# Kernel optimization log

Hardware: AMD Instinct MI355X
Metric: run time of the kernel (lower is better)

Reference implementation:

```python
import jax, jax.numpy as jnp
import numpy as np

N_HEAD = 16


def setup_inputs() -> dict:
    key = jax.random.key(0)
    ks = jax.random.split(key, 6)
    B, T, C = 8, 1024, 1024
    s = 0.02
    return {
        "x": jax.random.normal(ks[0], (B, T, C), dtype=jnp.float32),
        "Wk": jax.random.normal(ks[1], (C, C), dtype=jnp.float32) * s,
        "bk": jnp.zeros((C,), dtype=jnp.float32),
        "Wq": jax.random.normal(ks[2], (C, C), dtype=jnp.float32) * s,
        "bq": jnp.zeros((C,), dtype=jnp.float32),
        "Wv": jax.random.normal(ks[3], (C, C), dtype=jnp.float32) * s,
        "bv": jnp.zeros((C,), dtype=jnp.float32),
        "Wp": jax.random.normal(ks[4], (C, C), dtype=jnp.float32) * s,
        "bp": jnp.zeros((C,), dtype=jnp.float32),
    }


def reference(x, Wk, bk, Wq, bq, Wv, bv, Wp, bp):
    B, T, C = x.shape
    H = N_HEAD
    d = C // H
    # QKV projections, split heads -> [B, H, T, d]
    k = (x @ Wk + bk).reshape(B, T, H, d).transpose(0, 2, 1, 3)
    q = (x @ Wq + bq).reshape(B, T, H, d).transpose(0, 2, 1, 3)
    v = (x @ Wv + bv).reshape(B, T, H, d).transpose(0, 2, 1, 3)
    # NOTE: original computes K @ Q^T (not Q @ K^T) and scales by C^-0.5
    attn = jnp.einsum('bhid,bhjd->bhij', k, q) * (C ** -0.5)
    mask = jnp.tril(jnp.ones((T, T), dtype=bool))  # tril==0 positions masked
    attn = jnp.where(mask, attn, -jnp.inf)
    attn = jax.nn.softmax(attn, axis=-1)
    out = jnp.einsum('bhij,bhjd->bhid', attn, v)  # [B, H, T, d]
    out = out.transpose(0, 2, 1, 3).reshape(B, T, C)
    return out @ Wp + bp
```

## Files before the change

### kernel.cpp

```cpp
#include <hip/hip_runtime.h>

typedef unsigned short u16;
typedef unsigned int u32;
typedef __bf16 bf16x8 __attribute__((ext_vector_type(8)));
typedef float f32x4 __attribute__((ext_vector_type(4)));

__device__ __forceinline__ u16 f2bf(float f) {
  u32 u = __builtin_bit_cast(u32, f);
  u += 0x7fffu + ((u >> 16) & 1u);
  return (u16)(u >> 16);
}

#define GLOAD_LDS16(g, l) __builtin_amdgcn_global_load_lds( \
    (const __attribute__((address_space(1))) void*)(g),     \
    (__attribute__((address_space(3))) void*)(l), 16, 0, 0)

#define SCK (0.03125f * 1.44269504088896f)

#define BARF() do { asm volatile("" ::: "memory"); \
                    __builtin_amdgcn_s_barrier();  \
                    asm volatile("" ::: "memory"); } while (0)

__global__ __launch_bounds__(256) void cvt_x_k(const float* __restrict__ x,
                                               u16* __restrict__ xb) {
  size_t i = (size_t)blockIdx.x * 256 + threadIdx.x;
  const float4* p = reinterpret_cast<const float4*>(x) + i * 2;
  float4 a = p[0], b = p[1];
  u32 w0 = f2bf(a.x) | ((u32)f2bf(a.y) << 16);
  u32 w1 = f2bf(a.z) | ((u32)f2bf(a.w) << 16);
  u32 w2 = f2bf(b.x) | ((u32)f2bf(b.y) << 16);
  u32 w3 = f2bf(b.z) | ((u32)f2bf(b.w) << 16);
  uint4 o; o.x = w0; o.y = w1; o.z = w2; o.w = w3;
  *reinterpret_cast<uint4*>(xb + i * 8) = o;
}

__global__ __launch_bounds__(256) void transW_k(const float* __restrict__ W0,
                                                const float* __restrict__ W1,
                                                const float* __restrict__ W2,
                                                const float* __restrict__ W3,
                                                u16* __restrict__ WT) {
  __shared__ float tile[64][65];
  const float* W = blockIdx.z == 0 ? W0 : blockIdx.z == 1 ? W1
                 : blockIdx.z == 2 ? W2 : W3;
  u16* dst = WT + (size_t)blockIdx.z * 1024 * 1024;
  const int k0 = blockIdx.x * 64, n0 = blockIdx.y * 64;
  const int tid = threadIdx.x;
  const int rr = tid >> 4, c4 = (tid & 15) * 4;
#pragma unroll
  for (int p = 0; p < 4; ++p) {
    int r = rr + p * 16;
    float4 v = *reinterpret_cast<const float4*>(W + (size_t)(k0 + r) * 1024 + n0 + c4);
    tile[r][c4 + 0] = v.x; tile[r][c4 + 1] = v.y;
    tile[r][c4 + 2] = v.z; tile[r][c4 + 3] = v.w;
  }
  __syncthreads();
#pragma unroll
  for (int p = 0; p < 4; ++p) {
    int nl = rr + p * 16;
    u32 w0 = f2bf(tile[c4 + 0][nl]) | ((u32)f2bf(tile[c4 + 1][nl]) << 16);
    u32 w1 = f2bf(tile[c4 + 2][nl]) | ((u32)f2bf(tile[c4 + 3][nl]) << 16);
    uint2 o; o.x = w0; o.y = w1;
    *reinterpret_cast<uint2*>(dst + (size_t)(n0 + nl) * 1024 + k0 + c4) = o;
  }
}

template <int MODE>
__global__ __launch_bounds__(512, 2) void gemm8_k(
    const u16* __restrict__ A, const u16* __restrict__ BT,
    const float* __restrict__ bias0, const float* __restrict__ bias1,
    const float* __restrict__ bias2,
    u16* __restrict__ out_k, u16* __restrict__ out_q, u16* __restrict__ out_vT,
    float* __restrict__ out_f) {
  constexpr int BN = (MODE == 0) ? 192 : 128;
  constexpr int NB = BN / 64;
  constexpr int NBLO = NB - NB / 2;
  constexpr int NBHI = NB / 2;
  constexpr int LPT = 4 + NB;
  constexpr int WCW = BN / 4;

  __shared__ __align__(16) u16 As[2][256 * 64];
  __shared__ __align__(16) u16 Bs[2][BN * 64];

  const int tid = threadIdx.x;
  const int w = tid >> 6, lane = tid & 63;
  const int wr = w >> 2, wc = w & 3;
  const int fr = lane & 15, fq = lane >> 4;
  const int d = fr & 7;

  const int bid = (int)blockIdx.x;
  const int xcd = bid & 7, c = bid >> 3;
  int bx, by;
  if constexpr (MODE == 0) {
    bx = (xcd & 3) * 8 + (c >> 3);
    by = (xcd >> 2) * 8 + (c & 7);
  } else {
    bx = xcd * 4 + (c >> 3);
    by = c & 7;
  }
  const int row0 = bx * 256, col0 = by * BN;

  const int r0 = tid >> 3;
  const int cbg = (tid & 7) ^ (r0 & 7);
  const u16* Asrc = A + (size_t)(row0 + r0) * 1024 + cbg * 8;
  const u16* Bsrc = BT + (size_t)(col0 + r0) * 1024 + cbg * 8;

#define STAGE8(buf, t) do {                                                  \
    _Pragma("unroll")                                                        \
    for (int sw = 0; sw < 4; ++sw)                                           \
      GLOAD_LDS16(Asrc + (size_t)sw * 65536 + (t) * 64,                      \
                  &As[buf][sw * 4096 + tid * 8]);                            \
    _Pragma("unroll")                                                        \
    for (int sw = 0; sw < NB; ++sw)                                          \
      GLOAD_LDS16(Bsrc + (size_t)sw * 65536 + (t) * 64,                      \
                  &Bs[buf][sw * 4096 + tid * 8]);                            \
  } while (0)

#define AOFF(mb, kk) ((wr * 128 + (mb) * 16 + fr) * 128 + (((((kk) << 2) | fq) ^ d) << 4))
#define BOFF(nb, kk) ((wc * WCW + (nb) * 16 + fr) * 128 + (((((kk) << 2) | fq) ^ d) << 4))

  f32x4 acc[8][NB] = {};

  STAGE8(0, 0);
  STAGE8(1, 1);
  asm volatile("s_waitcnt vmcnt(%0)" :: "n"(LPT) : "memory");
  BARF();

#pragma unroll 1
  for (int g = 0; g < 16; ++g) {
    const int buf = g & 1;
    const char* Ac = (const char*)&As[buf][0];
    const char* Bc = (const char*)&Bs[buf][0];
    bf16x8 a03[4][2], a47[4][2], blo[NBLO][2], bhi[NBHI][2];

#pragma unroll
    for (int mb = 0; mb < 4; ++mb)
#pragma unroll
      for (int kk = 0; kk < 2; ++kk)
        a03[mb][kk] = *(const bf16x8*)(Ac + AOFF(mb, kk));
#pragma unroll
    for (int nb = 0; nb < NBLO; ++nb)
#pragma unroll
      for (int kk = 0; kk < 2; ++kk)
        blo[nb][kk] = *(const bf16x8*)(Bc + BOFF(nb, kk));
#pragma unroll
    for (int nb = 0; nb < NBHI; ++nb)
#pragma unroll
      for (int kk = 0; kk < 2; ++kk)
        bhi[nb][kk] = *(const bf16x8*)(Bc + BOFF(NBLO + nb, kk));
    asm volatile("s_waitcnt lgkmcnt(%0)" :: "n"(2 * NBHI) : "memory");
    __builtin_amdgcn_s_setprio(1);
#pragma unroll
    for (int mb = 0; mb < 4; ++mb)
#pragma unroll
      for (int nb = 0; nb < NBLO; ++nb)
#pragma unroll
        for (int kk = 0; kk < 2; ++kk)
          acc[mb][nb] = __builtin_amdgcn_mfma_f32_16x16x32_bf16(
              a03[mb][kk], blo[nb][kk], acc[mb][nb], 0, 0, 0);
    __builtin_amdgcn_s_setprio(0);
    BARF();

#pragma unroll
    for (int mb = 0; mb < 4; ++mb)
#pragma unroll
      for (int kk = 0; kk < 2; ++kk)
        a47[mb][kk] = *(const bf16x8*)(Ac + AOFF(4 + mb, kk));
    asm volatile("s_waitcnt lgkmcnt(8)" ::: "memory");
    __builtin_amdgcn_s_setprio(1);
#pragma unroll
    for (int mb = 0; mb < 4; ++mb)
#pragma unroll
      for (int nb = 0; nb < NBHI; ++nb)
#pragma unroll
        for (int kk = 0; kk < 2; ++kk)
          acc[mb][NBLO + nb] = __builtin_amdgcn_mfma_f32_16x16x32_bf16(
              a03[mb][kk], bhi[nb][kk], acc[mb][NBLO + nb], 0, 0, 0);
    __builtin_amdgcn_s_setprio(0);
    BARF();

    asm volatile("s_waitcnt lgkmcnt(0)" ::: "memory");
    __builtin_amdgcn_s_setprio(1);
#pragma unroll
    for (int mb = 0; mb < 4; ++mb)
#pragma unroll
      for (int nb = 0; nb < NBHI; ++nb)
#pragma unroll
        for (int kk = 0; kk < 2; ++kk)
          acc[4 + mb][NBLO + nb] = __builtin_amdgcn_mfma_f32_16x16x32_bf16(
              a47[mb][kk], bhi[nb][kk], acc[4 + mb][NBLO + nb], 0, 0, 0);
    __builtin_amdgcn_s_setprio(0);
    BARF();

    if (g + 2 < 16) STAGE8(buf, g + 2);
    __builtin_amdgcn_s_setprio(1);
#pragma unroll
    for (int mb = 0; mb < 4; ++mb)
#pragma unroll
      for (int nb = 0; nb < NBLO; ++nb)
#pragma unroll
        for (int kk = 0; kk < 2; ++kk)
          acc[4 + mb][nb] = __builtin_amdgcn_mfma_f32_16x16x32_bf16(
              a47[mb][kk], blo[nb][kk], acc[4 + mb][nb], 0, 0, 0);
    __builtin_amdgcn_s_setprio(0);
    if (g <= 13)      asm volatile("s_waitcnt vmcnt(%0)" :: "n"(LPT) : "memory");
    else if (g == 14) asm volatile("s_waitcnt vmcnt(0)" ::: "memory");
    BARF();
  }
#undef STAGE8
#undef AOFF
#undef BOFF

  if constexpr (MODE == 0) {
#pragma unroll
    for (int mb = 0; mb < 8; ++mb) {
#pragma unroll
      for (int nb = 0; nb < NB; ++nb) {
        const int rg = row0 + wr * 128 + mb * 16 + fq * 4;
        const int cg = col0 + wc * WCW + nb * 16 + fr;
        const int which = cg >> 10;
        const int nloc = cg & 1023;
        const float bv = (which == 0 ? bias0 : which == 1 ? bias1 : bias2)[nloc];
        if (which == 0) {
#pragma unroll
          for (int r = 0; r < 4; ++r)
            out_k[(size_t)(rg + r) * 1024 + nloc] = f2bf((acc[mb][nb][r] + bv) * SCK);
        } else if (which == 1) {
#pragma unroll
          for (int r = 0; r < 4; ++r)
            out_q[(size_t)(rg + r) * 1024 + nloc] = f2bf(acc[mb][nb][r] + bv);
        } else {
          const int bb = rg >> 10, t = rg & 1023;
          const int hh = nloc >> 6, dl = nloc & 63;
          u32 w0 = f2bf(acc[mb][nb][0] + bv) | ((u32)f2bf(acc[mb][nb][1] + bv) << 16);
          u32 w1 = f2bf(acc[mb][nb][2] + bv) | ((u32)f2bf(acc[mb][nb][3] + bv) << 16);
          uint2 ov; ov.x = w0; ov.y = w1;
          *reinterpret_cast<uint2*>(out_vT + ((size_t)(bb * 16 + hh) * 64 + dl) * 1024 + t) = ov;
        }
      }
    }
  } else {
#pragma unroll
    for (int mb = 0; mb < 8; ++mb)
#pragma unroll
      for (int nb = 0; nb < NB; ++nb) {
        const int rg = row0 + wr * 128 + mb * 16 + fq * 4;
        const int cg = col0 + wc * WCW + nb * 16 + fr;
        const float bv = bias0[cg];
#pragma unroll
        for (int r = 0; r < 4; ++r)
          out_f[(size_t)(rg + r) * 1024 + cg] = acc[mb][nb][r] + bv;
      }
  }
}

__global__ __launch_bounds__(256, 4) void attn_k(const u16* __restrict__ Q,
                                                 const u16* __restrict__ K,
                                                 const u16* __restrict__ vT,
                                                 u16* __restrict__ O) {
  __shared__ __align__(16) u16 KsA[4096], KsB[4096], VsA[4096], VsB[4096];
  __shared__ __align__(16) u16 Plds[4][16][40];
  const int tid = threadIdx.x;
  const int w = tid >> 6, lane = tid & 63;
  const int fr = lane & 15, fq = lane >> 4, koff = fq * 8;

  const int n = blockIdx.x + 8 * (blockIdx.y + 16 * blockIdx.z);
  const int xcd = n & 7, rest = n >> 3;
  const int g = rest >> 3, pair = rest & 7;
  const int hb = xcd + 8 * g;
  const int h = hb & 15, b = hb >> 4;

  const size_t bstride = (size_t)1024 * 1024;
  const u16* Qb = Q + b * bstride + h * 64;
  const u16* Kg = K + b * bstride + h * 64;
  const u16* Vg = vT + ((size_t)(b * 16 + h) * 64) * 1024;

  const int srow = tid >> 3;
  const int scb = (tid & 7) ^ (srow & 7);
  const u16* KgT = Kg + (size_t)srow * 1024 + scb * 8;
  const u16* VgT = Vg + (size_t)srow * 1024 + scb * 8;

  const int vK0 = fr * 128 + ((fq ^ (fr & 7)) << 4);
  const int vK1 = vK0 ^ 64;
  const int pw = w * 1280 + fq * 320 + fr * 2;
  const int pr = w * 1280 + fr * 80 + fq * 16;

#define STAGE(KS, VS, jt) do {                                          \
    GLOAD_LDS16(KgT + (size_t)(jt) * 65536, &KS[tid * 8]);              \
    GLOAD_LDS16(KgT + (size_t)(jt) * 65536 + 32 * 1024, &KS[2048 + tid * 8]); \
    GLOAD_LDS16(VgT + (jt) * 64, &VS[tid * 8]);                         \
    GLOAD_LDS16(VgT + (jt) * 64 + 32 * 1024, &VS[2048 + tid * 8]);      \
  } while (0)

#pragma unroll 1
  for (int ph = 0; ph < 2; ++ph) {
    const int T = ph ? (15 - pair) : pair;
    const int i0 = T * 64;
    const int ibase = i0 + w * 16;

    bf16x8 aq0 = *reinterpret_cast<const bf16x8*>(&Qb[(size_t)(ibase + fr) * 1024 + koff]);
    bf16x8 aq1 = *reinterpret_cast<const bf16x8*>(&Qb[(size_t)(ibase + fr) * 1024 + koff + 32]);

    f32x4 o[4] = {};
    float lp[4] = {0.f, 0.f, 0.f, 0.f};

    auto compute = [&](const u16* KS, const u16* VS, bool diag) {
      const char* Kc = reinterpret_cast<const char*>(KS);
      const char* Vc = reinterpret_cast<const char*>(VS);
      f32x4 s[4];
#pragma unroll
      for (int jc = 0; jc < 4; ++jc) {
        bf16x8 bk0 = *reinterpret_cast<const bf16x8*>(Kc + vK0 + jc * 2048);
        bf16x8 bk1 = *reinterpret_cast<const bf16x8*>(Kc + vK1 + jc * 2048);
        f32x4 z = {};
        z = __builtin_amdgcn_mfma_f32_16x16x32_bf16(aq0, bk0, z, 0, 0, 0);
        s[jc] = __builtin_amdgcn_mfma_f32_16x16x32_bf16(aq1, bk1, z, 0, 0, 0);
      }
      bf16x8 bv0[4], bv1[4];
#pragma unroll
      for (int dn = 0; dn < 4; ++dn) {
        bv0[dn] = *reinterpret_cast<const bf16x8*>(Vc + vK0 + dn * 2048);
        bv1[dn] = *reinterpret_cast<const bf16x8*>(Vc + vK1 + dn * 2048);
      }
      float p[4][4];
      if (diag) {
#pragma unroll
        for (int r = 0; r < 4; ++r) {
          const int il = w * 16 + fq * 4 + r;
#pragma unroll
          for (int jc = 0; jc < 4; ++jc) {
            const int jl = jc * 16 + fr;
            p[jc][r] = (jl <= il) ? __builtin_amdgcn_exp2f(s[jc][r]) : 0.f;
          }
        }
      } else {
#pragma unroll
        for (int r = 0; r < 4; ++r)
#pragma unroll
          for (int jc = 0; jc < 4; ++jc)
            p[jc][r] = __builtin_amdgcn_exp2f(s[jc][r]);
      }
#pragma unroll
      for (int r = 0; r < 4; ++r)
        lp[r] += (p[0][r] + p[1][r]) + (p[2][r] + p[3][r]);
      char* Pc = reinterpret_cast<char*>(&Plds[0][0][0]);
#pragma unroll
      for (int jh = 0; jh < 2; ++jh) {
#pragma unroll
        for (int r = 0; r < 4; ++r)
#pragma unroll
          for (int j2 = 0; j2 < 2; ++j2)
            *reinterpret_cast<u16*>(Pc + pw + r * 80 + j2 * 32) = f2bf(p[jh * 2 + j2][r]);
        bf16x8 ap = *reinterpret_cast<const bf16x8*>(Pc + pr);
#pragma unroll
        for (int dn = 0; dn < 4; ++dn)
          o[dn] = __builtin_amdgcn_mfma_f32_16x16x32_bf16(ap, jh ? bv1[dn] : bv0[dn],
                                                          o[dn], 0, 0, 0);
      }
    };

    STAGE(KsA, VsA, 0);
    int t = 0;
    while (true) {
      {
        const bool more = t < T;
        if (more) STAGE(KsB, VsB, t + 1);
        if (more) { asm volatile("s_waitcnt vmcnt(4)" ::: "memory"); }
        else      { asm volatile("s_waitcnt vmcnt(0)" ::: "memory"); }
        __builtin_amdgcn_s_barrier();
        compute(KsA, VsA, t == T);
        __builtin_amdgcn_s_barrier();
        if (!more) break;
        ++t;
      }
      {
        const bool more = t < T;
        if (more) STAGE(KsA, VsA, t + 1);
        if (more) { asm volatile("s_waitcnt vmcnt(4)" ::: "memory"); }
        else      { asm volatile("s_waitcnt vmcnt(0)" ::: "memory"); }
        __builtin_amdgcn_s_barrier();
        compute(KsB, VsB, t == T);
        __builtin_amdgcn_s_barrier();
        if (!more) break;
        ++t;
      }
    }

#pragma unroll
    for (int x = 1; x < 16; x <<= 1)
#pragma unroll
      for (int r = 0; r < 4; ++r) lp[r] += __shfl_xor(lp[r], x);
#pragma unroll
    for (int r = 0; r < 4; ++r) {
      const float inv = 1.f / lp[r];
      const int ig = ibase + fq * 4 + r;
#pragma unroll
      for (int dn = 0; dn < 4; ++dn)
        O[((size_t)b * 1024 + ig) * 1024 + h * 64 + dn * 16 + fr] = f2bf(o[dn][r] * inv);
    }
  }
#undef STAGE
}

extern "C" void kernel_launch(void* const* d_in, const int* in_sizes, int n_in,
                              void* d_out, int out_size, void* d_ws, size_t ws_size,
                              hipStream_t stream) {
  const float* x  = (const float*)d_in[0];
  const float* Wk = (const float*)d_in[1];
  const float* bk = (const float*)d_in[2];
  const float* Wq = (const float*)d_in[3];
  const float* bq = (const float*)d_in[4];
  const float* Wv = (const float*)d_in[5];
  const float* bv = (const float*)d_in[6];
  const float* Wp = (const float*)d_in[7];
  const float* bp = (const float*)d_in[8];
  float* out = (float*)d_out;

  char* ws = (char*)d_ws;
  u16* xb   = (u16*)(ws);
  u16* WT   = (u16*)(ws + ((size_t)16 << 20));
  u16* kbuf = (u16*)(ws + ((size_t)24 << 20));
  u16* qbuf = (u16*)(ws + ((size_t)40 << 20));
  u16* vT   = (u16*)(ws + ((size_t)56 << 20));
  u16* aout = (u16*)(ws + ((size_t)72 << 20));

  cvt_x_k<<<4096, 256, 0, stream>>>(x, xb);
  transW_k<<<dim3(16, 16, 4), 256, 0, stream>>>(Wk, Wq, Wv, Wp, WT);
  gemm8_k<0><<<512, 512, 0, stream>>>(xb, WT, bk, bq, bv,
                                      kbuf, qbuf, vT, nullptr);
  attn_k<<<dim3(8, 16, 8), 256, 0, stream>>>(kbuf, qbuf, vT, aout);
  gemm8_k<1><<<256, 512, 0, stream>>>(aout, WT + (size_t)3 * 1024 * 1024,
                                      bp, nullptr, nullptr,
                                      nullptr, nullptr, nullptr, out);
}
```

Before: 138.4 us.

## Merge prep kernels into one launch and reorder GEMM MFMA phases by k-slice

Combines the x-to-bf16 conversion and weight transpose kernels into a single launch, using the block index to pick which job a block does. This removes one kernel launch and its gap. It also restructures the GEMM inner loop so each of the four barrier-separated phases covers a full k-half (kk=0 or kk=1) across all N blocks rather than splitting into lo/hi N halves. The new LDS load order and lgkmcnt waits are meant to overlap the fragment loads with the MFMAs differently, at the risk of longer stalls or higher register pressure.

```diff
diff --git a/kernel.cpp b/kernel.cpp
--- a/kernel.cpp
+++ b/kernel.cpp
@@ -21,30 +21,32 @@
                     __builtin_amdgcn_s_barrier();  \
                     asm volatile("" ::: "memory"); } while (0)
 
-__global__ __launch_bounds__(256) void cvt_x_k(const float* __restrict__ x,
-                                               u16* __restrict__ xb) {
-  size_t i = (size_t)blockIdx.x * 256 + threadIdx.x;
-  const float4* p = reinterpret_cast<const float4*>(x) + i * 2;
-  float4 a = p[0], b = p[1];
-  u32 w0 = f2bf(a.x) | ((u32)f2bf(a.y) << 16);
-  u32 w1 = f2bf(a.z) | ((u32)f2bf(a.w) << 16);
-  u32 w2 = f2bf(b.x) | ((u32)f2bf(b.y) << 16);
-  u32 w3 = f2bf(b.z) | ((u32)f2bf(b.w) << 16);
-  uint4 o; o.x = w0; o.y = w1; o.z = w2; o.w = w3;
-  *reinterpret_cast<uint4*>(xb + i * 8) = o;
-}
-
-__global__ __launch_bounds__(256) void transW_k(const float* __restrict__ W0,
-                                                const float* __restrict__ W1,
-                                                const float* __restrict__ W2,
-                                                const float* __restrict__ W3,
-                                                u16* __restrict__ WT) {
+__global__ __launch_bounds__(256) void prep_k(const float* __restrict__ x,
+                                              const float* __restrict__ W0,
+                                              const float* __restrict__ W1,
+                                              const float* __restrict__ W2,
+                                              const float* __restrict__ W3,
+                                              u16* __restrict__ xb,
+                                              u16* __restrict__ WT) {
   __shared__ float tile[64][65];
-  const float* W = blockIdx.z == 0 ? W0 : blockIdx.z == 1 ? W1
-                 : blockIdx.z == 2 ? W2 : W3;
-  u16* dst = WT + (size_t)blockIdx.z * 1024 * 1024;
-  const int k0 = blockIdx.x * 64, n0 = blockIdx.y * 64;
   const int tid = threadIdx.x;
+  if (blockIdx.x < 4096) {
+    size_t i = (size_t)blockIdx.x * 256 + tid;
+    const float4* p = reinterpret_cast<const float4*>(x) + i * 2;
+    float4 a = p[0], b = p[1];
+    u32 w0 = f2bf(a.x) | ((u32)f2bf(a.y) << 16);
+    u32 w1 = f2bf(a.z) | ((u32)f2bf(a.w) << 16);
+    u32 w2 = f2bf(b.x) | ((u32)f2bf(b.y) << 16);
+    u32 w3 = f2bf(b.z) | ((u32)f2bf(b.w) << 16);
+    uint4 o; o.x = w0; o.y = w1; o.z = w2; o.w = w3;
+    *reinterpret_cast<uint4*>(xb + i * 8) = o;
+    return;
+  }
+  const int bid2 = blockIdx.x - 4096;
+  const int z = bid2 >> 8, kt = bid2 & 15, nt = (bid2 >> 4) & 15;
+  const float* W = z == 0 ? W0 : z == 1 ? W1 : z == 2 ? W2 : W3;
+  u16* dst = WT + (size_t)z * 1024 * 1024;
+  const int k0 = kt * 64, n0 = nt * 64;
   const int rr = tid >> 4, c4 = (tid & 15) * 4;
 #pragma unroll
   for (int p = 0; p < 4; ++p) {
@@ -73,8 +75,6 @@
     float* __restrict__ out_f) {
   constexpr int BN = (MODE == 0) ? 192 : 128;
   constexpr int NB = BN / 64;
-  constexpr int NBLO = NB - NB / 2;
-  constexpr int NBHI = NB / 2;
   constexpr int LPT = 4 + NB;
   constexpr int WCW = BN / 4;
 
@@ -130,65 +130,52 @@
     const int buf = g & 1;
     const char* Ac = (const char*)&As[buf][0];
     const char* Bc = (const char*)&Bs[buf][0];
-    bf16x8 a03[4][2], a47[4][2], blo[NBLO][2], bhi[NBHI][2];
-
+    bf16x8 a03[4][2], a47[4][2], b[NB][2];
+
+#pragma unroll
+    for (int mb = 0; mb < 4; ++mb) a03[mb][0] = *(const bf16x8*)(Ac + AOFF(mb, 0));
+#pragma unroll
+    for (int nb = 0; nb < NB; ++nb) b[nb][0] = *(const bf16x8*)(Bc + BOFF(nb, 0));
+#pragma unroll
+    for (int nb = 0; nb < NB; ++nb) b[nb][1] = *(const bf16x8*)(Bc + BOFF(nb, 1));
+#pragma unroll
+    for (int mb = 0; mb < 4; ++mb) a03[mb][1] = *(const bf16x8*)(Ac + AOFF(mb, 1));
+    asm volatile("s_waitcnt lgkmcnt(%0)" :: "n"(NB + 4) : "memory");
+    __builtin_amdgcn_s_setprio(1);
 #pragma unroll
     for (int mb = 0; mb < 4; ++mb)
 #pragma unroll
-      for (int kk = 0; kk < 2; ++kk)
-        a03[mb][kk] = *(const bf16x8*)(Ac + AOFF(mb, kk));
-#pragma unroll
-    for (int nb = 0; nb < NBLO; ++nb)
-#pragma unroll
-      for (int kk = 0; kk < 2; ++kk)
-        blo[nb][kk] = *(const bf16x8*)(Bc + BOFF(nb, kk));
-#pragma unroll
-    for (int nb = 0; nb < NBHI; ++nb)
-#pragma unroll
-      for (int kk = 0; kk < 2; ++kk)
-        bhi[nb][kk] = *(const bf16x8*)(Bc + BOFF(NBLO + nb, kk));
-    asm volatile("s_waitcnt lgkmcnt(%0)" :: "n"(2 * NBHI) : "memory");
-    __builtin_amdgcn_s_setprio(1);
-#pragma unroll
-    for (int mb = 0; mb < 4; ++mb)
-#pragma unroll
-      for (int nb = 0; nb < NBLO; ++nb)
-#pragma unroll
-        for (int kk = 0; kk < 2; ++kk)
-          acc[mb][nb] = __builtin_amdgcn_mfma_f32_16x16x32_bf16(
-              a03[mb][kk], blo[nb][kk], acc[mb][nb], 0, 0, 0);
+      for (int nb = 0; nb < NB; ++nb)
+        acc[mb][nb] = __builtin_amdgcn_mfma_f32_16x16x32_bf16(
+            a03[mb][0], b[nb][0], acc[mb][nb], 0, 0, 0);
     __builtin_amdgcn_s_setprio(0);
     BARF();
 
+    asm volatile("s_waitcnt lgkmcnt(0)" ::: "memory");
+    __builtin_amdgcn_s_setprio(1);
 #pragma unroll
     for (int mb = 0; mb < 4; ++mb)
 #pragma unroll
-      for (int kk = 0; kk < 2; ++kk)
-        a47[mb][kk] = *(const bf16x8*)(Ac + AOFF(4 + mb, kk));
-    asm volatile("s_waitcnt lgkmcnt(8)" ::: "memory");
-    __builtin_amdgcn_s_setprio(1);
-#pragma unroll
-    for (int mb = 0; mb < 4; ++mb)
-#pragma unroll
-      for (int nb = 0; nb < NBHI; ++nb)
-#pragma unroll
-        for (int kk = 0; kk < 2; ++kk)
-          acc[mb][NBLO + nb] = __builtin_amdgcn_mfma_f32_16x16x32_bf16(
-              a03[mb][kk], bhi[nb][kk], acc[mb][NBLO + nb], 0, 0, 0);
+      for (int nb = 0; nb < NB; ++nb)
+        acc[mb][nb] = __builtin_amdgcn_mfma_f32_16x16x32_bf16(
+            a03[mb][1], b[nb][1], acc[mb][nb], 0, 0, 0);
     __builtin_amdgcn_s_setprio(0);
     BARF();
 
+#pragma unroll
+    for (int mb = 0; mb < 4; ++mb) a47[mb][0] = *(const bf16x8*)(Ac + AOFF(4 + mb, 0));
+#pragma unroll
+    for (int mb = 0; mb < 4; ++mb) a47[mb][1] = *(const bf16x8*)(Ac + AOFF(4 + mb, 1));
+    asm volatile("s_waitcnt lgkmcnt(4)" ::: "memory");
+    __builtin_amdgcn_s_setprio(1);
+#pragma unroll
+    for (int mb = 0; mb < 4; ++mb)
+#pragma unroll
+      for (int nb = 0; nb < NB; ++nb)
+        acc[4 + mb][nb] = __builtin_amdgcn_mfma_f32_16x16x32_bf16(
+            a47[mb][0], b[nb][0], acc[4 + mb][nb], 0, 0, 0);
+    __builtin_amdgcn_s_setprio(0);
     asm volatile("s_waitcnt lgkmcnt(0)" ::: "memory");
-    __builtin_amdgcn_s_setprio(1);
-#pragma unroll
-    for (int mb = 0; mb < 4; ++mb)
-#pragma unroll
-      for (int nb = 0; nb < NBHI; ++nb)
-#pragma unroll
-        for (int kk = 0; kk < 2; ++kk)
-          acc[4 + mb][NBLO + nb] = __builtin_amdgcn_mfma_f32_16x16x32_bf16(
-              a47[mb][kk], bhi[nb][kk], acc[4 + mb][NBLO + nb], 0, 0, 0);
-    __builtin_amdgcn_s_setprio(0);
     BARF();
 
     if (g + 2 < 16) STAGE8(buf, g + 2);
@@ -196,11 +183,9 @@
 #pragma unroll
     for (int mb = 0; mb < 4; ++mb)
 #pragma unroll
-      for (int nb = 0; nb < NBLO; ++nb)
-#pragma unroll
-        for (int kk = 0; kk < 2; ++kk)
-          acc[4 + mb][nb] = __builtin_amdgcn_mfma_f32_16x16x32_bf16(
-              a47[mb][kk], blo[nb][kk], acc[4 + mb][nb], 0, 0, 0);
+      for (int nb = 0; nb < NB; ++nb)
+        acc[4 + mb][nb] = __builtin_amdgcn_mfma_f32_16x16x32_bf16(
+            a47[mb][1], b[nb][1], acc[4 + mb][nb], 0, 0, 0);
     __builtin_amdgcn_s_setprio(0);
     if (g <= 13)      asm volatile("s_waitcnt vmcnt(%0)" :: "n"(LPT) : "memory");
     else if (g == 14) asm volatile("s_waitcnt vmcnt(0)" ::: "memory");
@@ -423,8 +408,7 @@
   u16* vT   = (u16*)(ws + ((size_t)56 << 20));
   u16* aout = (u16*)(ws + ((size_t)72 << 20));
 
-  cvt_x_k<<<4096, 256, 0, stream>>>(x, xb);
-  transW_k<<<dim3(16, 16, 4), 256, 0, stream>>>(Wk, Wq, Wv, Wp, WT);
+  prep_k<<<5120, 256, 0, stream>>>(x, Wk, Wq, Wv, Wp, xb, WT);
   gemm8_k<0><<<512, 512, 0, stream>>>(xb, WT, bk, bq, bv,
                                       kbuf, qbuf, vT, nullptr);
   attn_k<<<dim3(8, 16, 8), 256, 0, stream>>>(kbuf, qbuf, vT, aout);
```

Measured after the change: 139.9 us. About the same (+1.1%).
